# Performance work log

Measured on AMD Instinct MI355X. Metric: run time of the kernel, lower is better.

The kernel has to match this reference:

```python
import jax, jax.numpy as jnp
import numpy as np
from itertools import product

B = 2
X, Y, Z = 96, 96, 192          # voxel grid (x, y, t)
NPB = 300_000                   # occupied voxels per batch item
PX, PY, PZ = X // 2, Y // 2, Z // 4  # pooled grid (kernel/stride [2,2,4])
CIN, COUT, KVOL, NCONV = 32, 64, 27, 2
EPS = 1e-5


def _build_maps():
    """Builds sparse coordinates, maxpool segment ids and 3x3x3 conv kernel maps
    (gather/scatter index pairs per kernel offset), mirroring MinkowskiEngine's
    coordinate manager."""
    rng = np.random.default_rng(0)
    coords = []
    for b in range(B):
        lin = rng.choice(X * Y * Z, NPB, replace=False)
        x = lin // (Y * Z)
        y = (lin // Z) % Y
        z = lin % Z
        coords.append(np.stack([np.full(NPB, b), x, y, z], 1))
    c = np.concatenate(coords).astype(np.int64)  # [N,4] (b,x,y,z)
    # max-pool coord map: out coord = (x//2, y//2, z//4)
    pk = ((c[:, 0] * PX + c[:, 1] // 2) * PY + c[:, 2] // 2) * PZ + c[:, 3] // 4
    uniq, inv = np.unique(pk, return_inverse=True)
    M = len(uniq)
    pz = uniq % PZ
    py = (uniq // PZ) % PY
    px = (uniq // (PZ * PY)) % PX
    pb = uniq // (PZ * PY * PX)
    lut = np.full(B * PX * PY * PZ, -1, np.int64)
    lut[uniq] = np.arange(M)
    ins, outs = [], []
    for dx, dy, dz in product((-1, 0, 1), repeat=3):
        nx, ny, nz = px + dx, py + dy, pz + dz
        ok = (nx >= 0) & (nx < PX) & (ny >= 0) & (ny < PY) & (nz >= 0) & (nz < PZ)
        nk = ((pb * PX + np.clip(nx, 0, PX - 1)) * PY + np.clip(ny, 0, PY - 1)) * PZ + np.clip(nz, 0, PZ - 1)
        j = np.where(ok, lut[nk], -1)
        sel = j >= 0
        ins.append(j[sel])
        outs.append(np.arange(M)[sel])
    L = max(len(a) for a in ins)
    ci = np.full((KVOL, L), M, np.int64)  # pad -> index M (zero row)
    co = np.full((KVOL, L), M, np.int64)  # pad -> dummy out row M (dropped)
    for k in range(KVOL):
        ci[k, : len(ins[k])] = ins[k]
        co[k, : len(outs[k])] = outs[k]
    return inv.astype(np.int64), ci, co, M


def setup_inputs() -> dict:
    key = jax.random.key(0)
    ks = jax.random.split(key, 4)
    pool_seg, ci, co, M = _build_maps()
    N = B * NPB
    feats = jax.random.normal(ks[0], (N, CIN), jnp.float32)
    Wd = jax.random.normal(ks[1], (CIN, COUT), jnp.float32) / np.sqrt(CIN)
    W1 = jax.random.normal(ks[2], (KVOL, COUT, COUT), jnp.float32) / np.sqrt(KVOL * COUT)
    W2 = jax.random.normal(ks[3], (KVOL, COUT, COUT), jnp.float32) / np.sqrt(KVOL * COUT)
    ones = jnp.ones((COUT,), jnp.float32)
    zeros = jnp.zeros((COUT,), jnp.float32)
    return {
        "feats": feats, "Wd": Wd,
        "g0": ones, "b0": zeros,
        "W1": W1, "g1": ones, "b1": zeros,
        "W2": W2, "g2": ones, "b2": zeros,
        "pool_seg": jnp.asarray(pool_seg),
        "conv_in": jnp.asarray(ci), "conv_out": jnp.asarray(co),
        "num_pooled": int(M),
    }


def _bn(h, g, b):
    # training-mode batch norm over all sparse points (biased variance, eps=1e-5)
    m = h.mean(0)
    v = jnp.mean((h - m) ** 2, 0)
    return (h - m) * (g / jnp.sqrt(v + EPS)) + b


def _sparse_conv(h, W, conv_in, conv_out, M):
    # gather-GEMM-scatter over 27 kernel offsets (MinkowskiConvolution, bias=False)
    C = W.shape[-1]
    hp = jnp.concatenate([h, jnp.zeros((1, h.shape[1]), h.dtype)])  # zero pad row
    out = jnp.zeros((M + 1, C), h.dtype)
    for k in range(W.shape[0]):
        out = out.at[conv_out[k]].add(hp[conv_in[k]] @ W[k])
    return out[:M]


def reference(feats, Wd, g0, b0, W1, g1, b1, W2, g2, b2,
              pool_seg, conv_in, conv_out, num_pooled):
    # down_conv (1x1, bias=False) -> BN -> ELU
    h = jax.nn.elu(_bn(feats @ Wd, g0, b0))
    # MinkowskiMaxPooling kernel=stride=[2,2,4] == segment max over pooled cells
    down = jax.ops.segment_max(h, pool_seg, num_segments=num_pooled)
    # nConvs LUConv blocks: ELU(BN(conv3x3x3(x)))
    o = down
    for W, g, b in ((W1, g1, b1), (W2, g2, b2)):
        o = jax.nn.elu(_bn(_sparse_conv(o, W, conv_in, conv_out, num_pooled), g, b))
    # residual add + ELU
    return jax.nn.elu(o + down)
```

## Files before the change

kernel.cpp:

```cpp
#include <hip/hip_runtime.h>
#include <math.h>

#define CIN  32
#define COUT 64
#define KVOL 27
#define EPSF 1e-5f

typedef __attribute__((ext_vector_type(8))) short          short8;
typedef __attribute__((ext_vector_type(8))) unsigned short u16x8;
typedef __attribute__((ext_vector_type(4))) float          float4v;

__device__ __forceinline__ float eluf(float x) { return x > 0.f ? x : expm1f(x); }

__device__ __forceinline__ unsigned short f2bf(float x) {
    unsigned u = __float_as_uint(x);
    unsigned r = (u + 0x7FFFu + ((u >> 16) & 1u)) >> 16;
    return (unsigned short)r;
}
__device__ __forceinline__ unsigned pk2bf(float lo, float hi) {
    return (unsigned)f2bf(lo) | ((unsigned)f2bf(hi) << 16);
}
__device__ __forceinline__ float bf2f(unsigned short h) {
    return __uint_as_float(((unsigned)h) << 16);
}

__global__ void cvt_w_kernel(const float* __restrict__ W1, const float* __restrict__ W2,
                             const float* __restrict__ Wd,
                             unsigned short* __restrict__ Wt1, unsigned short* __restrict__ Wt2,
                             unsigned short* __restrict__ Wdt)
{
    int b = blockIdx.x;
    int t = threadIdx.x;
    if (b == 54) {
        for (int e = t; e < CIN * COUT; e += 256) {
            int i = e >> 6, c = e & 63;
            Wdt[c * CIN + i] = f2bf(Wd[e]);
        }
        return;
    }
    const float* W = (b < 27) ? W1 : W2;
    unsigned short* Wt = (b < 27) ? Wt1 : Wt2;
    int k = (b < 27) ? b : b - 27;
    const float* src = W + (size_t)k * (COUT * COUT);
    unsigned short* dst = Wt + (size_t)k * (COUT * COUT);
    for (int e = t; e < COUT * COUT; e += 256) {
        int i = e >> 6, c = e & 63;
        dst[c * COUT + i] = f2bf(src[e]);
    }
}

__global__ __launch_bounds__(256) void gemm_t_kernel(
    const float* __restrict__ feats, const unsigned short* __restrict__ Wdt,
    int N, unsigned short* __restrict__ t_bf, float* __restrict__ red0)
{
    __shared__ float red_s[64];
    __shared__ float red_q[64];
    int t = threadIdx.x;
    if (t < 64) { red_s[t] = 0.f; red_q[t] = 0.f; }
    __syncthreads();

    int w = t >> 6, lane = t & 63, l15 = lane & 15, quad = lane >> 4;

    short8 aw[4];
    #pragma unroll
    for (int mt = 0; mt < 4; ++mt)
        aw[mt] = *(const short8*)(Wdt + (size_t)(16 * mt + l15) * CIN + quad * 8);

    float s1[16], sq[16];
    #pragma unroll
    for (int e = 0; e < 16; ++e) { s1[e] = 0.f; sq[e] = 0.f; }

    int numTiles = (N + 15) >> 4;
    int stride = gridDim.x * 4;
    int tile = blockIdx.x * 4 + w;

    float4 c0 = make_float4(0.f, 0.f, 0.f, 0.f), c1 = c0;
    {
        int pt = tile * 16 + l15;
        if (tile < numTiles && pt < N) {
            const float4* s = (const float4*)(feats + (size_t)pt * CIN + quad * 8);
            c0 = s[0]; c1 = s[1];
        }
    }

    while (tile < numTiles) {
        int nt = tile + stride;
        float4 n0 = make_float4(0.f, 0.f, 0.f, 0.f), n1 = n0;
        {
            int npt = nt * 16 + l15;
            if (nt < numTiles && npt < N) {
                const float4* s = (const float4*)(feats + (size_t)npt * CIN + quad * 8);
                n0 = s[0]; n1 = s[1];
            }
        }
        union { short8 v; unsigned u[4]; } b;
        b.u[0] = pk2bf(c0.x, c0.y);
        b.u[1] = pk2bf(c0.z, c0.w);
        b.u[2] = pk2bf(c1.x, c1.y);
        b.u[3] = pk2bf(c1.z, c1.w);

        float4v acc[4];
        #pragma unroll
        for (int mt = 0; mt < 4; ++mt)
            acc[mt] = __builtin_amdgcn_mfma_f32_16x16x32_bf16(
                aw[mt], b.v, (float4v){0.f, 0.f, 0.f, 0.f}, 0, 0, 0);

        int pt = tile * 16 + l15;
        if (pt < N) {
            #pragma unroll
            for (int mt = 0; mt < 4; ++mt) {
                uint2 o;
                o.x = pk2bf(acc[mt][0], acc[mt][1]);
                o.y = pk2bf(acc[mt][2], acc[mt][3]);
                *(uint2*)(t_bf + (size_t)pt * COUT + mt * 16 + quad * 4) = o;
            }
        }
        #pragma unroll
        for (int mt = 0; mt < 4; ++mt)
            #pragma unroll
            for (int e = 0; e < 4; ++e) {
                float v = acc[mt][e];
                s1[mt * 4 + e] += v; sq[mt * 4 + e] += v * v;
            }
        c0 = n0; c1 = n1;
        tile = nt;
    }

    #pragma unroll
    for (int m = 1; m <= 8; m <<= 1) {
        #pragma unroll
        for (int e = 0; e < 16; ++e) {
            s1[e] += __shfl_xor(s1[e], m);
            sq[e] += __shfl_xor(sq[e], m);
        }
    }
    if (l15 == 0) {
        #pragma unroll
        for (int e = 0; e < 16; ++e) {
            int ch = (e >> 2) * 16 + quad * 4 + (e & 3);
            atomicAdd(&red_s[ch], s1[e]);
            atomicAdd(&red_q[ch], sq[e]);
        }
    }
    __syncthreads();
    float* dst = red0 + (size_t)(blockIdx.x & 3) * 128;
    if (t < 64)       atomicAdd(&dst[t], red_s[t]);
    else if (t < 128) atomicAdd(&dst[t], red_q[t - 64]);
}

__global__ void fin0_kernel(const float* __restrict__ red, const float* __restrict__ g,
                            const float* __restrict__ b, float* __restrict__ scale,
                            float* __restrict__ shift, int cnt)
{
    int c = threadIdx.x;
    float s = 0.f, q = 0.f;
    #pragma unroll
    for (int i = 0; i < 4; ++i) { s += red[i * 128 + c]; q += red[i * 128 + 64 + c]; }
    float m = s / (float)cnt;
    float var = q / (float)cnt - m * m;
    float sc = g[c] / sqrtf(var + EPSF);
    scale[c] = sc;
    shift[c] = b[c] - m * sc;
}

__global__ void bucket_kernel(const int* __restrict__ pool_seg,
                              int* __restrict__ cnt, int* __restrict__ bucket, int N)
{
    int j = blockIdx.x * 256 + threadIdx.x;
    if (j < N) {
        int s = pool_seg[j];
        int pos = atomicAdd(&cnt[s], 1);
        bucket[(size_t)s * 16 + pos] = j;
    }
}

__global__ __launch_bounds__(256) void pool_max_kernel(
    const unsigned short* __restrict__ t_bf,
    const int* __restrict__ cnt, const int* __restrict__ bucket,
    const float* __restrict__ scale0, const float* __restrict__ shift0,
    unsigned short* __restrict__ down_bf, int M)
{
    int id = blockIdx.x * 256 + threadIdx.x;
    int s = id >> 4, cg = id & 15;
    if (s >= M) return;
    int n = cnt[s];
    const int4* bk4 = (const int4*)(bucket + (size_t)s * 16);
    float4 mx = make_float4(-INFINITY, -INFINITY, -INFINITY, -INFINITY);
    float4 mn = make_float4( INFINITY,  INFINITY,  INFINITY,  INFINITY);
    #pragma unroll
    for (int ch = 0; ch < 4; ++ch) {
        if (ch * 4 >= n) break;
        int4 b4 = bk4[ch];
        #pragma unroll
        for (int e = 0; e < 4; ++e) {
            int p = ch * 4 + e;
            if (p < n) {
                int idx = (e == 0) ? b4.x : (e == 1) ? b4.y : (e == 2) ? b4.z : b4.w;
                ushort4 v = *(const ushort4*)(t_bf + (size_t)idx * COUT + cg * 4);
                float f0 = bf2f(v.x), f1 = bf2f(v.y), f2 = bf2f(v.z), f3 = bf2f(v.w);
                mx.x = fmaxf(mx.x, f0); mn.x = fminf(mn.x, f0);
                mx.y = fmaxf(mx.y, f1); mn.y = fminf(mn.y, f1);
                mx.z = fmaxf(mx.z, f2); mn.z = fminf(mn.z, f2);
                mx.w = fmaxf(mx.w, f3); mn.w = fminf(mn.w, f3);
            }
        }
    }
    int c0 = cg * 4;
    float4 sc = *(const float4*)(scale0 + c0);
    float4 sh = *(const float4*)(shift0 + c0);
    ushort4 o;
    o.x = f2bf(eluf(sc.x * (sc.x >= 0.f ? mx.x : mn.x) + sh.x));
    o.y = f2bf(eluf(sc.y * (sc.y >= 0.f ? mx.y : mn.y) + sh.y));
    o.z = f2bf(eluf(sc.z * (sc.z >= 0.f ? mx.z : mn.z) + sh.z));
    o.w = f2bf(eluf(sc.w * (sc.w >= 0.f ? mx.w : mn.w) + sh.w));
    *(ushort4*)(down_bf + (size_t)s * COUT + c0) = o;
}

__global__ void nbr_kernel(const int* __restrict__ conv_out, const int* __restrict__ conv_in,
                           int* __restrict__ nbrT, int L, int M)
{
    int k = blockIdx.y;
    int idx = blockIdx.x * 256 + threadIdx.x;
    if (idx < L) {
        int e = k * L + idx;
        int j = conv_out[e];
        if (j < M) nbrT[(size_t)k * M + j] = conv_in[e];
    }
}

__global__ void bn_elu_cvt_kernel(const float* __restrict__ o1,
                                  const float* __restrict__ scale,
                                  const float* __restrict__ shift,
                                  unsigned short* __restrict__ o1t, int n)
{
    int i = blockIdx.x * 256 + threadIdx.x;
    if (i < n) {
        int c = i & 63;
        o1t[i] = f2bf(eluf(o1[i] * scale[c] + shift[c]));
    }
}

__global__ __launch_bounds__(256) void conv_mfma_kernel(
    const unsigned short* __restrict__ in, const unsigned short* __restrict__ Wt,
    const int* __restrict__ nbrT, int M,
    float* __restrict__ out, float* __restrict__ red)
{
    __shared__ __align__(16) unsigned short A_lds[128 * 72];
    __shared__ __align__(16) unsigned short W_lds[64 * 72];
    __shared__ float red_s[64];
    __shared__ float red_q[64];
    int t = threadIdx.x;
    int base = blockIdx.x * 128;
    int w = t >> 6, lane = t & 63, l15 = lane & 15, quad = lane >> 4;

    if (t < 64) { red_s[t] = 0.f; red_q[t] = 0.f; }

    float4v acc[2][4];
    #pragma unroll
    for (int s = 0; s < 2; ++s)
        #pragma unroll
        for (int n = 0; n < 4; ++n)
            acc[s][n] = (float4v){0.f, 0.f, 0.f, 0.f};

    int ar = t >> 1, ah = t & 1;
    int gj = base + ar;
    int wc = t >> 2, wq = t & 3;

    for (int k = 0; k < KVOL; ++k) {
        __syncthreads();
        {
            int idx = (gj < M) ? nbrT[(size_t)k * M + gj] : -1;
            u16x8 c0 = {0,0,0,0,0,0,0,0}, c1 = c0, c2 = c0, c3 = c0;
            if (idx >= 0) {
                const u16x8* src = (const u16x8*)(in + (size_t)idx * COUT + 32 * ah);
                c0 = src[0]; c1 = src[1]; c2 = src[2]; c3 = src[3];
            }
            u16x8* dst = (u16x8*)(A_lds + ar * 72 + 32 * ah);
            dst[0] = c0; dst[1] = c1; dst[2] = c2; dst[3] = c3;
        }
        {
            const u16x8* src = (const u16x8*)(Wt + (size_t)k * (COUT * COUT) + wc * COUT + 16 * wq);
            u16x8* dst = (u16x8*)(W_lds + wc * 72 + 16 * wq);
            dst[0] = src[0]; dst[1] = src[1];
        }
        __syncthreads();
        #pragma unroll
        for (int kk = 0; kk < 64; kk += 32) {
            short8 a0 = *(const short8*)(A_lds + (32 * w + l15) * 72 + kk + quad * 8);
            short8 a1 = *(const short8*)(A_lds + (32 * w + 16 + l15) * 72 + kk + quad * 8);
            #pragma unroll
            for (int n = 0; n < 4; ++n) {
                short8 b = *(const short8*)(W_lds + (16 * n + l15) * 72 + kk + quad * 8);
                acc[0][n] = __builtin_amdgcn_mfma_f32_16x16x32_bf16(a0, b, acc[0][n], 0, 0, 0);
                acc[1][n] = __builtin_amdgcn_mfma_f32_16x16x32_bf16(a1, b, acc[1][n], 0, 0, 0);
            }
        }
    }

    #pragma unroll
    for (int s = 0; s < 2; ++s) {
        int row = base + 32 * w + 16 * s + quad * 4;
        #pragma unroll
        for (int n = 0; n < 4; ++n) {
            int c = 16 * n + l15;
            #pragma unroll
            for (int e = 0; e < 4; ++e)
                if (row + e < M) out[(size_t)(row + e) * COUT + c] = acc[s][n][e];
        }
    }
    #pragma unroll
    for (int n = 0; n < 4; ++n) {
        float s1 = 0.f, sq = 0.f;
        #pragma unroll
        for (int s = 0; s < 2; ++s)
            #pragma unroll
            for (int e = 0; e < 4; ++e) { float v = acc[s][n][e]; s1 += v; sq += v * v; }
        s1 += __shfl_xor(s1, 16); sq += __shfl_xor(sq, 16);
        s1 += __shfl_xor(s1, 32); sq += __shfl_xor(sq, 32);
        if (quad == 0) {
            atomicAdd(&red_s[16 * n + l15], s1);
            atomicAdd(&red_q[16 * n + l15], sq);
        }
    }
    __syncthreads();
    if (t < 64)       atomicAdd(&red[t], red_s[t]);
    else if (t < 128) atomicAdd(&red[t], red_q[t - 64]);
}

__global__ void finC_kernel(const float* __restrict__ red, const float* __restrict__ g,
                            const float* __restrict__ b, float* __restrict__ scale,
                            float* __restrict__ shift, int M)
{
    int c = threadIdx.x;
    float m = red[c] / (float)M;
    float var = red[64 + c] / (float)M - m * m;
    float sc = g[c] / sqrtf(var + EPSF);
    scale[c] = sc;
    shift[c] = b[c] - m * sc;
}

__global__ void final_kernel(float* __restrict__ out, const unsigned short* __restrict__ down_bf,
                             const float* __restrict__ scale2, const float* __restrict__ shift2,
                             int n)
{
    int i = blockIdx.x * 256 + threadIdx.x;
    if (i < n) {
        int c = i & 63;
        float y = eluf(out[i] * scale2[c] + shift2[c]);
        out[i] = eluf(y + bf2f(down_bf[i]));
    }
}

extern "C" void kernel_launch(void* const* d_in, const int* in_sizes, int n_in,
                              void* d_out, int out_size, void* d_ws, size_t ws_size,
                              hipStream_t stream)
{
    (void)n_in; (void)ws_size;
    const float* feats    = (const float*)d_in[0];
    const float* Wd       = (const float*)d_in[1];
    const float* g0       = (const float*)d_in[2];
    const float* b0       = (const float*)d_in[3];
    const float* W1       = (const float*)d_in[4];
    const float* g1       = (const float*)d_in[5];
    const float* b1       = (const float*)d_in[6];
    const float* W2       = (const float*)d_in[7];
    const float* g2       = (const float*)d_in[8];
    const float* b2       = (const float*)d_in[9];
    const int*   pool_seg = (const int*)d_in[10];
    const int*   conv_in  = (const int*)d_in[11];
    const int*   conv_out = (const int*)d_in[12];

    int N = in_sizes[0] / CIN;
    int M = out_size / COUT;
    int L = in_sizes[11] / KVOL;

    char* ws = (char*)d_ws;
    size_t off = 0;
    auto alloc = [&](size_t bytes) -> void* {
        void* p = ws + off;
        off = (off + bytes + 255) & ~(size_t)255;
        return p;
    };
    float*          o1      = (float*)alloc((size_t)M * COUT * 4);
    unsigned short* down_bf = (unsigned short*)alloc((size_t)M * COUT * 2);
    unsigned short* o1t     = (unsigned short*)alloc((size_t)M * COUT * 2);
    unsigned short* t_bf    = (unsigned short*)alloc((size_t)N * COUT * 2);
    int*            nbrT    = (int*)alloc((size_t)KVOL * M * 4);
    unsigned short* Wt1     = (unsigned short*)alloc((size_t)KVOL * COUT * COUT * 2);
    unsigned short* Wt2     = (unsigned short*)alloc((size_t)KVOL * COUT * COUT * 2);
    unsigned short* Wdt     = (unsigned short*)alloc((size_t)CIN * COUT * 2);
    int*            cnt     = (int*)alloc((size_t)M * 4);
    int*            bucket  = (int*)alloc((size_t)M * 16 * 4);
    float* red  = (float*)alloc((size_t)768 * 4);
    float* red0 = red, *red1 = red + 512, *red2 = red + 640;
    float* sreg = (float*)alloc((size_t)6 * 64 * 4);
    float* scale0 = sreg, *shift0 = sreg + 64;
    float* scale1 = sreg + 128, *shift1 = sreg + 192;
    float* scale2 = sreg + 256, *shift2 = sreg + 320;

    hipMemsetAsync(nbrT, 0xFF, (size_t)KVOL * M * 4, stream);
    hipMemsetAsync(cnt, 0, (size_t)M * 4, stream);
    hipMemsetAsync(red, 0, (size_t)768 * 4, stream);

    cvt_w_kernel<<<55, 256, 0, stream>>>(W1, W2, Wd, Wt1, Wt2, Wdt);
    gemm_t_kernel<<<1024, 256, 0, stream>>>(feats, Wdt, N, t_bf, red0);
    fin0_kernel<<<1, 64, 0, stream>>>(red0, g0, b0, scale0, shift0, N);
    bucket_kernel<<<(N + 255) / 256, 256, 0, stream>>>(pool_seg, cnt, bucket, N);
    pool_max_kernel<<<(M * 16 + 255) / 256, 256, 0, stream>>>(
        t_bf, cnt, bucket, scale0, shift0, down_bf, M);
    dim3 gn((L + 255) / 256, KVOL);
    nbr_kernel<<<gn, 256, 0, stream>>>(conv_out, conv_in, nbrT, L, M);

    int cblocks = (M + 127) / 128;
    conv_mfma_kernel<<<cblocks, 256, 0, stream>>>(down_bf, Wt1, nbrT, M, o1, red1);
    finC_kernel<<<1, 64, 0, stream>>>(red1, g1, b1, scale1, shift1, M);
    bn_elu_cvt_kernel<<<(M * COUT + 255) / 256, 256, 0, stream>>>(o1, scale1, shift1, o1t, M * COUT);
    conv_mfma_kernel<<<cblocks, 256, 0, stream>>>(o1t, Wt2, nbrT, M, (float*)d_out, red2);
    finC_kernel<<<1, 64, 0, stream>>>(red2, g2, b2, scale2, shift2, M);
    final_kernel<<<(M * COUT + 255) / 256, 256, 0, stream>>>(
        (float*)d_out, down_bf, scale2, shift2, M * COUT);
}
```

Measured before the change: 551.0 us.

## Restructure sparse conv: point-major neighbor table, register gathers, bf16 intermediates

The sparse conv kernel now uses a point-major neighbor table (28 ints per point) loaded once into registers. Each lane gathers its own point's features straight into MFMA B operands and prefetches the next offset, so the A-tile LDS staging is gone. Weights are double-buffered in LDS, leaving one barrier per kernel offset, and blocks shrink to 64 points with BN stats reduced through shuffles into four partial slots. Conv outputs are stored as bf16 rather than fp32 and the elementwise kernels are vectorized, which cuts memory traffic but adds rounding before batch norm.

```diff
diff --git a/kernel.cpp b/kernel.cpp
--- a/kernel.cpp
+++ b/kernel.cpp
@@ -148,9 +148,9 @@
     else if (t < 128) atomicAdd(&dst[t], red_q[t - 64]);
 }
 
-__global__ void fin0_kernel(const float* __restrict__ red, const float* __restrict__ g,
-                            const float* __restrict__ b, float* __restrict__ scale,
-                            float* __restrict__ shift, int cnt)
+__global__ void fin_kernel(const float* __restrict__ red, const float* __restrict__ g,
+                           const float* __restrict__ b, float* __restrict__ scale,
+                           float* __restrict__ shift, int cnt)
 {
     int c = threadIdx.x;
     float s = 0.f, q = 0.f;
@@ -217,137 +217,170 @@
 }
 
 __global__ void nbr_kernel(const int* __restrict__ conv_out, const int* __restrict__ conv_in,
-                           int* __restrict__ nbrT, int L, int M)
+                           int* __restrict__ nbr, int L, int M)
 {
     int k = blockIdx.y;
     int idx = blockIdx.x * 256 + threadIdx.x;
     if (idx < L) {
         int e = k * L + idx;
         int j = conv_out[e];
-        if (j < M) nbrT[(size_t)k * M + j] = conv_in[e];
-    }
-}
-
-__global__ void bn_elu_cvt_kernel(const float* __restrict__ o1,
+        if (j < M) nbr[(size_t)j * 28 + k] = conv_in[e];
+    }
+}
+
+__global__ void bn_elu_cvt_kernel(const unsigned short* __restrict__ in,
                                   const float* __restrict__ scale,
                                   const float* __restrict__ shift,
-                                  unsigned short* __restrict__ o1t, int n)
+                                  unsigned short* __restrict__ out, int n4)
 {
     int i = blockIdx.x * 256 + threadIdx.x;
-    if (i < n) {
-        int c = i & 63;
-        o1t[i] = f2bf(eluf(o1[i] * scale[c] + shift[c]));
+    if (i < n4) {
+        int c0 = (i * 4) & 63;
+        ushort4 v = ((const ushort4*)in)[i];
+        float4 sc = *(const float4*)(scale + c0);
+        float4 sh = *(const float4*)(shift + c0);
+        ushort4 o;
+        o.x = f2bf(eluf(bf2f(v.x) * sc.x + sh.x));
+        o.y = f2bf(eluf(bf2f(v.y) * sc.y + sh.y));
+        o.z = f2bf(eluf(bf2f(v.z) * sc.z + sh.z));
+        o.w = f2bf(eluf(bf2f(v.w) * sc.w + sh.w));
+        ((ushort4*)out)[i] = o;
     }
 }
 
 __global__ __launch_bounds__(256) void conv_mfma_kernel(
     const unsigned short* __restrict__ in, const unsigned short* __restrict__ Wt,
-    const int* __restrict__ nbrT, int M,
-    float* __restrict__ out, float* __restrict__ red)
-{
-    __shared__ __align__(16) unsigned short A_lds[128 * 72];
-    __shared__ __align__(16) unsigned short W_lds[64 * 72];
+    const int* __restrict__ nbr, int M,
+    unsigned short* __restrict__ out_bf, float* __restrict__ red)
+{
+    __shared__ __align__(16) unsigned short W_lds[2][64 * 72];
     __shared__ float red_s[64];
     __shared__ float red_q[64];
     int t = threadIdx.x;
-    int base = blockIdx.x * 128;
     int w = t >> 6, lane = t & 63, l15 = lane & 15, quad = lane >> 4;
-
     if (t < 64) { red_s[t] = 0.f; red_q[t] = 0.f; }
 
-    float4v acc[2][4];
-    #pragma unroll
-    for (int s = 0; s < 2; ++s)
-        #pragma unroll
-        for (int n = 0; n < 4; ++n)
-            acc[s][n] = (float4v){0.f, 0.f, 0.f, 0.f};
-
-    int ar = t >> 1, ah = t & 1;
-    int gj = base + ar;
+    int pt = blockIdx.x * 64 + w * 16 + l15;
+
+    int idx[28];
+    if (pt < M) {
+        const int4* src = (const int4*)(nbr + (size_t)pt * 28);
+        #pragma unroll
+        for (int q = 0; q < 7; ++q) {
+            int4 v = src[q];
+            idx[q * 4 + 0] = v.x; idx[q * 4 + 1] = v.y;
+            idx[q * 4 + 2] = v.z; idx[q * 4 + 3] = v.w;
+        }
+    } else {
+        #pragma unroll
+        for (int e = 0; e < 28; ++e) idx[e] = -1;
+    }
+
     int wc = t >> 2, wq = t & 3;
+    {
+        const u16x8* src = (const u16x8*)(Wt + wc * COUT + 16 * wq);
+        u16x8* dst = (u16x8*)(&W_lds[0][wc * 72 + 16 * wq]);
+        dst[0] = src[0]; dst[1] = src[1];
+    }
+
+    float4v acc[4];
+    #pragma unroll
+    for (int mt = 0; mt < 4; ++mt) acc[mt] = (float4v){0.f, 0.f, 0.f, 0.f};
+
+    short8 b0c = {0,0,0,0,0,0,0,0}, b1c = b0c;
+    {
+        int ix = idx[0];
+        if (ix >= 0) {
+            b0c = *(const short8*)(in + (size_t)ix * COUT + quad * 8);
+            b1c = *(const short8*)(in + (size_t)ix * COUT + 32 + quad * 8);
+        }
+    }
+    __syncthreads();
 
     for (int k = 0; k < KVOL; ++k) {
+        if (k + 1 < KVOL) {
+            const u16x8* src = (const u16x8*)(Wt + (size_t)(k + 1) * (COUT * COUT)
+                                              + wc * COUT + 16 * wq);
+            u16x8* dst = (u16x8*)(&W_lds[(k + 1) & 1][wc * 72 + 16 * wq]);
+            dst[0] = src[0]; dst[1] = src[1];
+        }
+        short8 b0n = {0,0,0,0,0,0,0,0}, b1n = b0n;
+        if (k + 1 < KVOL) {
+            int ix = idx[k + 1];
+            if (ix >= 0) {
+                b0n = *(const short8*)(in + (size_t)ix * COUT + quad * 8);
+                b1n = *(const short8*)(in + (size_t)ix * COUT + 32 + quad * 8);
+            }
+        }
+        const unsigned short* wl = W_lds[k & 1];
+        #pragma unroll
+        for (int mt = 0; mt < 4; ++mt) {
+            short8 a0 = *(const short8*)(wl + (16 * mt + l15) * 72 + quad * 8);
+            short8 a1 = *(const short8*)(wl + (16 * mt + l15) * 72 + 32 + quad * 8);
+            acc[mt] = __builtin_amdgcn_mfma_f32_16x16x32_bf16(a0, b0c, acc[mt], 0, 0, 0);
+            acc[mt] = __builtin_amdgcn_mfma_f32_16x16x32_bf16(a1, b1c, acc[mt], 0, 0, 0);
+        }
+        b0c = b0n; b1c = b1n;
         __syncthreads();
-        {
-            int idx = (gj < M) ? nbrT[(size_t)k * M + gj] : -1;
-            u16x8 c0 = {0,0,0,0,0,0,0,0}, c1 = c0, c2 = c0, c3 = c0;
-            if (idx >= 0) {
-                const u16x8* src = (const u16x8*)(in + (size_t)idx * COUT + 32 * ah);
-                c0 = src[0]; c1 = src[1]; c2 = src[2]; c3 = src[3];
-            }
-            u16x8* dst = (u16x8*)(A_lds + ar * 72 + 32 * ah);
-            dst[0] = c0; dst[1] = c1; dst[2] = c2; dst[3] = c3;
-        }
-        {
-            const u16x8* src = (const u16x8*)(Wt + (size_t)k * (COUT * COUT) + wc * COUT + 16 * wq);
-            u16x8* dst = (u16x8*)(W_lds + wc * 72 + 16 * wq);
-            dst[0] = src[0]; dst[1] = src[1];
-        }
-        __syncthreads();
-        #pragma unroll
-        for (int kk = 0; kk < 64; kk += 32) {
-            short8 a0 = *(const short8*)(A_lds + (32 * w + l15) * 72 + kk + quad * 8);
-            short8 a1 = *(const short8*)(A_lds + (32 * w + 16 + l15) * 72 + kk + quad * 8);
-            #pragma unroll
-            for (int n = 0; n < 4; ++n) {
-                short8 b = *(const short8*)(W_lds + (16 * n + l15) * 72 + kk + quad * 8);
-                acc[0][n] = __builtin_amdgcn_mfma_f32_16x16x32_bf16(a0, b, acc[0][n], 0, 0, 0);
-                acc[1][n] = __builtin_amdgcn_mfma_f32_16x16x32_bf16(a1, b, acc[1][n], 0, 0, 0);
-            }
-        }
-    }
-
-    #pragma unroll
-    for (int s = 0; s < 2; ++s) {
-        int row = base + 32 * w + 16 * s + quad * 4;
-        #pragma unroll
-        for (int n = 0; n < 4; ++n) {
-            int c = 16 * n + l15;
-            #pragma unroll
-            for (int e = 0; e < 4; ++e)
-                if (row + e < M) out[(size_t)(row + e) * COUT + c] = acc[s][n][e];
-        }
-    }
-    #pragma unroll
-    for (int n = 0; n < 4; ++n) {
-        float s1 = 0.f, sq = 0.f;
-        #pragma unroll
-        for (int s = 0; s < 2; ++s)
-            #pragma unroll
-            for (int e = 0; e < 4; ++e) { float v = acc[s][n][e]; s1 += v; sq += v * v; }
-        s1 += __shfl_xor(s1, 16); sq += __shfl_xor(sq, 16);
-        s1 += __shfl_xor(s1, 32); sq += __shfl_xor(sq, 32);
-        if (quad == 0) {
-            atomicAdd(&red_s[16 * n + l15], s1);
-            atomicAdd(&red_q[16 * n + l15], sq);
+    }
+
+    if (pt < M) {
+        #pragma unroll
+        for (int mt = 0; mt < 4; ++mt) {
+            uint2 o;
+            o.x = pk2bf(acc[mt][0], acc[mt][1]);
+            o.y = pk2bf(acc[mt][2], acc[mt][3]);
+            *(uint2*)(out_bf + (size_t)pt * COUT + mt * 16 + quad * 4) = o;
+        }
+    }
+    float s1[16], sq[16];
+    #pragma unroll
+    for (int mt = 0; mt < 4; ++mt)
+        #pragma unroll
+        for (int e = 0; e < 4; ++e) {
+            float v = acc[mt][e];
+            s1[mt * 4 + e] = v; sq[mt * 4 + e] = v * v;
+        }
+    #pragma unroll
+    for (int m = 1; m <= 8; m <<= 1) {
+        #pragma unroll
+        for (int e = 0; e < 16; ++e) {
+            s1[e] += __shfl_xor(s1[e], m);
+            sq[e] += __shfl_xor(sq[e], m);
+        }
+    }
+    if (l15 == 0) {
+        #pragma unroll
+        for (int e = 0; e < 16; ++e) {
+            int ch = (e >> 2) * 16 + quad * 4 + (e & 3);
+            atomicAdd(&red_s[ch], s1[e]);
+            atomicAdd(&red_q[ch], sq[e]);
         }
     }
     __syncthreads();
-    if (t < 64)       atomicAdd(&red[t], red_s[t]);
-    else if (t < 128) atomicAdd(&red[t], red_q[t - 64]);
-}
-
-__global__ void finC_kernel(const float* __restrict__ red, const float* __restrict__ g,
-                            const float* __restrict__ b, float* __restrict__ scale,
-                            float* __restrict__ shift, int M)
-{
-    int c = threadIdx.x;
-    float m = red[c] / (float)M;
-    float var = red[64 + c] / (float)M - m * m;
-    float sc = g[c] / sqrtf(var + EPSF);
-    scale[c] = sc;
-    shift[c] = b[c] - m * sc;
-}
-
-__global__ void final_kernel(float* __restrict__ out, const unsigned short* __restrict__ down_bf,
+    float* dst = red + (size_t)(blockIdx.x & 3) * 128;
+    if (t < 64)       atomicAdd(&dst[t], red_s[t]);
+    else if (t < 128) atomicAdd(&dst[t], red_q[t - 64]);
+}
+
+__global__ void final_kernel(const unsigned short* __restrict__ raw,
+                             const unsigned short* __restrict__ down_bf,
                              const float* __restrict__ scale2, const float* __restrict__ shift2,
-                             int n)
+                             float* __restrict__ out, int n4)
 {
     int i = blockIdx.x * 256 + threadIdx.x;
-    if (i < n) {
-        int c = i & 63;
-        float y = eluf(out[i] * scale2[c] + shift2[c]);
-        out[i] = eluf(y + bf2f(down_bf[i]));
+    if (i < n4) {
+        int c0 = (i * 4) & 63;
+        ushort4 r = ((const ushort4*)raw)[i];
+        ushort4 d = ((const ushort4*)down_bf)[i];
+        float4 sc = *(const float4*)(scale2 + c0);
+        float4 sh = *(const float4*)(shift2 + c0);
+        float4 o;
+        o.x = eluf(eluf(bf2f(r.x) * sc.x + sh.x) + bf2f(d.x));
+        o.y = eluf(eluf(bf2f(r.y) * sc.y + sh.y) + bf2f(d.y));
+        o.z = eluf(eluf(bf2f(r.z) * sc.z + sh.z) + bf2f(d.z));
+        o.w = eluf(eluf(bf2f(r.w) * sc.w + sh.w) + bf2f(d.w));
+        ((float4*)out)[i] = o;
     }
 }
 
@@ -381,42 +414,44 @@
         off = (off + bytes + 255) & ~(size_t)255;
         return p;
     };
-    float*          o1      = (float*)alloc((size_t)M * COUT * 4);
     unsigned short* down_bf = (unsigned short*)alloc((size_t)M * COUT * 2);
+    unsigned short* o1_bf   = (unsigned short*)alloc((size_t)M * COUT * 2);
     unsigned short* o1t     = (unsigned short*)alloc((size_t)M * COUT * 2);
+    unsigned short* o2_bf   = (unsigned short*)alloc((size_t)M * COUT * 2);
     unsigned short* t_bf    = (unsigned short*)alloc((size_t)N * COUT * 2);
-    int*            nbrT    = (int*)alloc((size_t)KVOL * M * 4);
+    int*            nbr     = (int*)alloc((size_t)M * 28 * 4);
     unsigned short* Wt1     = (unsigned short*)alloc((size_t)KVOL * COUT * COUT * 2);
     unsigned short* Wt2     = (unsigned short*)alloc((size_t)KVOL * COUT * COUT * 2);
     unsigned short* Wdt     = (unsigned short*)alloc((size_t)CIN * COUT * 2);
     int*            cnt     = (int*)alloc((size_t)M * 4);
     int*            bucket  = (int*)alloc((size_t)M * 16 * 4);
-    float* red  = (float*)alloc((size_t)768 * 4);
-    float* red0 = red, *red1 = red + 512, *red2 = red + 640;
+    float* red  = (float*)alloc((size_t)1536 * 4);
+    float* red0 = red, *red1 = red + 512, *red2 = red + 1024;
     float* sreg = (float*)alloc((size_t)6 * 64 * 4);
     float* scale0 = sreg, *shift0 = sreg + 64;
     float* scale1 = sreg + 128, *shift1 = sreg + 192;
     float* scale2 = sreg + 256, *shift2 = sreg + 320;
 
-    hipMemsetAsync(nbrT, 0xFF, (size_t)KVOL * M * 4, stream);
+    hipMemsetAsync(nbr, 0xFF, (size_t)M * 28 * 4, stream);
     hipMemsetAsync(cnt, 0, (size_t)M * 4, stream);
-    hipMemsetAsync(red, 0, (size_t)768 * 4, stream);
+    hipMemsetAsync(red, 0, (size_t)1536 * 4, stream);
 
     cvt_w_kernel<<<55, 256, 0, stream>>>(W1, W2, Wd, Wt1, Wt2, Wdt);
     gemm_t_kernel<<<1024, 256, 0, stream>>>(feats, Wdt, N, t_bf, red0);
-    fin0_kernel<<<1, 64, 0, stream>>>(red0, g0, b0, scale0, shift0, N);
+    fin_kernel<<<1, 64, 0, stream>>>(red0, g0, b0, scale0, shift0, N);
     bucket_kernel<<<(N + 255) / 256, 256, 0, stream>>>(pool_seg, cnt, bucket, N);
     pool_max_kernel<<<(M * 16 + 255) / 256, 256, 0, stream>>>(
         t_bf, cnt, bucket, scale0, shift0, down_bf, M);
     dim3 gn((L + 255) / 256, KVOL);
-    nbr_kernel<<<gn, 256, 0, stream>>>(conv_out, conv_in, nbrT, L, M);
-
-    int cblocks = (M + 127) / 128;
-    conv_mfma_kernel<<<cblocks, 256, 0, stream>>>(down_bf, Wt1, nbrT, M, o1, red1);
-    finC_kernel<<<1, 64, 0, stream>>>(red1, g1, b1, scale1, shift1, M);
-    bn_elu_cvt_kernel<<<(M * COUT + 255) / 256, 256, 0, stream>>>(o1, scale1, shift1, o1t, M * COUT);
-    conv_mfma_kernel<<<cblocks, 256, 0, stream>>>(o1t, Wt2, nbrT, M, (float*)d_out, red2);
-    finC_kernel<<<1, 64, 0, stream>>>(red2, g2, b2, scale2, shift2, M);
-    final_kernel<<<(M * COUT + 255) / 256, 256, 0, stream>>>(
-        (float*)d_out, down_bf, scale2, shift2, M * COUT);
-}
+    nbr_kernel<<<gn, 256, 0, stream>>>(conv_out, conv_in, nbr, L, M);
+
+    int cblocks = (M + 63) / 64;
+    int n4 = M * COUT / 4;
+    conv_mfma_kernel<<<cblocks, 256, 0, stream>>>(down_bf, Wt1, nbr, M, o1_bf, red1);
+    fin_kernel<<<1, 64, 0, stream>>>(red1, g1, b1, scale1, shift1, M);
+    bn_elu_cvt_kernel<<<(n4 + 255) / 256, 256, 0, stream>>>(o1_bf, scale1, shift1, o1t, n4);
+    conv_mfma_kernel<<<cblocks, 256, 0, stream>>>(o1t, Wt2, nbr, M, o2_bf, red2);
+    fin_kernel<<<1, 64, 0, stream>>>(red2, g2, b2, scale2, shift2, M);
+    final_kernel<<<(n4 + 255) / 256, 256, 0, stream>>>(
+        o2_bf, down_bf, scale2, shift2, (float*)d_out, n4);
+}
```

Measured after the change: 629.3 us. 1.14x slower.
